# Kernel tuning notes

Measured on AMD Instinct MI355X. Metric: run time of the kernel, lower is better.

Reference implementation:

```python
import jax, jax.numpy as jnp
import numpy as np

B = 4; C = 3; IMG = 256; P = 16; HP = 16; HW = 256
DIM = 512; DEPTH = 6; HEADS = 8; DH = 64
NS = 50; SH = 4; SDH = 64; ITERS = 3; RPD = 128; FF = 2048; N = NS + HW


def _ln(x, g, b):
    m = jnp.mean(x, -1, keepdims=True)
    v = jnp.var(x, -1, keepdims=True)
    return (x - m) * jax.lax.rsqrt(v + 1e-5) * g + b


def _rms(x, g):
    # lucidrains RMSNorm: F.normalize(x, dim=-1) * sqrt(dim) * gamma
    n = jnp.linalg.norm(x, axis=-1, keepdims=True)
    return x / jnp.maximum(n, 1e-12) * (DIM ** 0.5) * g


def setup_inputs() -> dict:
    key = jax.random.key(0)
    ks = iter(jax.random.split(key, 64))
    def W(*s):
        return jax.random.normal(next(ks), s, jnp.float32) * 0.02
    SI = SH * SDH
    d = {}
    d['images'] = jax.random.normal(next(ks), (B, C, IMG, IMG), jnp.float32)
    d['slot_noise'] = jax.random.normal(next(ks), (B, NS, DIM), jnp.float32)
    d['patch_w'] = W(C * P * P, DIM); d['patch_b'] = jnp.zeros((DIM,))
    d['hpos'] = W(HP, DIM); d['wpos'] = W(HP, DIM)
    d['rp_w1'] = W(2, RPD); d['rp_b1'] = jnp.zeros((RPD,))
    d['rp_w2'] = W(RPD, RPD); d['rp_b2'] = jnp.zeros((RPD,))
    d['rp_w3'] = W(RPD, HEADS); d['rp_b3'] = jnp.zeros((HEADS,))
    d['slots_mu'] = W(1, 1, DIM); d['slots_logsigma'] = jnp.zeros((1, 1, DIM))
    d['sa_ln_in_g'] = jnp.ones((DIM,)); d['sa_ln_in_b'] = jnp.zeros((DIM,))
    d['sa_ln_sl_g'] = jnp.ones((DIM,)); d['sa_ln_sl_b'] = jnp.zeros((DIM,))
    d['sa_wq'] = W(DIM, SI); d['sa_bq'] = jnp.zeros((SI,))
    d['sa_wk'] = W(DIM, SI); d['sa_bk'] = jnp.zeros((SI,))
    d['sa_wv'] = W(DIM, SI); d['sa_bv'] = jnp.zeros((SI,))
    d['sa_wo'] = W(SI, DIM); d['sa_bo'] = jnp.zeros((DIM,))
    d['gru_wih'] = W(DIM, 3 * DIM); d['gru_whh'] = W(DIM, 3 * DIM)
    d['gru_bih'] = jnp.zeros((3 * DIM,)); d['gru_bhh'] = jnp.zeros((3 * DIM,))
    d['sa_ln_ff_g'] = jnp.ones((DIM,)); d['sa_ln_ff_b'] = jnp.zeros((DIM,))
    d['sa_mlp_w1'] = W(DIM, DIM); d['sa_mlp_b1'] = jnp.zeros((DIM,))
    d['sa_mlp_w2'] = W(DIM, DIM); d['sa_mlp_b2'] = jnp.zeros((DIM,))
    d['s2c_w'] = W(DIM, 2); d['s2c_b'] = jnp.zeros((2,))
    d['attn_g'] = jnp.ones((DEPTH, DIM))
    d['wq'] = W(DEPTH, DIM, HEADS * DH); d['wk'] = W(DEPTH, DIM, HEADS * DH)
    d['wv'] = W(DEPTH, DIM, HEADS * DH); d['wo'] = W(DEPTH, HEADS * DH, DIM)
    d['ff_g'] = jnp.ones((DEPTH, DIM))
    d['ff_w1'] = W(DEPTH, DIM, FF); d['ff_b1'] = jnp.zeros((DEPTH, FF))
    d['ff_w2'] = W(DEPTH, FF, DIM); d['ff_b2'] = jnp.zeros((DEPTH, DIM))
    d['final_g'] = jnp.ones((DIM,))
    d['pred_w'] = W(DIM, DIM); d['pred_b'] = jnp.zeros((DIM,))
    return d


def reference(images, slot_noise, patch_w, patch_b, hpos, wpos,
              rp_w1, rp_b1, rp_w2, rp_b2, rp_w3, rp_b3,
              slots_mu, slots_logsigma, sa_ln_in_g, sa_ln_in_b, sa_ln_sl_g, sa_ln_sl_b,
              sa_wq, sa_bq, sa_wk, sa_bk, sa_wv, sa_bv, sa_wo, sa_bo,
              gru_wih, gru_whh, gru_bih, gru_bhh, sa_ln_ff_g, sa_ln_ff_b,
              sa_mlp_w1, sa_mlp_b1, sa_mlp_w2, sa_mlp_b2, s2c_w, s2c_b,
              attn_g, wq, wk, wv, wo, ff_g, ff_w1, ff_b1, ff_w2, ff_b2,
              final_g, pred_w, pred_b):
    b = images.shape[0]
    # patchify: b c (h p1) (w p2) -> b h w (p1 p2 c)
    x = images.reshape(b, C, HP, P, HP, P).transpose(0, 2, 4, 3, 5, 1).reshape(b, HP, HP, P * P * C)
    tokens = x @ patch_w + patch_b                     # [b, HP, HP, DIM]
    tokens = tokens + hpos[:, None, :] + wpos[None, :, :]
    tokens = tokens.reshape(b, HW, DIM)
    # --- multi-head slot attention ---
    inp = _ln(tokens, sa_ln_in_g, sa_ln_in_b)
    k = (inp @ sa_wk + sa_bk).reshape(b, HW, SH, SDH).transpose(0, 2, 1, 3)
    v = (inp @ sa_wv + sa_bv).reshape(b, HW, SH, SDH).transpose(0, 2, 1, 3)
    slots = slots_mu + jnp.exp(slots_logsigma) * slot_noise  # [b, NS, DIM]
    scale = SDH ** -0.5
    for _ in range(ITERS):
        prev = slots
        s = _ln(slots, sa_ln_sl_g, sa_ln_sl_b)
        q = (s @ sa_wq + sa_bq).reshape(b, NS, SH, SDH).transpose(0, 2, 1, 3)
        dots = jnp.einsum('bhid,bhjd->bhij', q, k) * scale     # [b, SH, NS, HW]
        attn = jax.nn.softmax(dots, axis=-2) + 1e-8            # softmax over slots
        attn = attn / jnp.sum(attn, -1, keepdims=True)         # weighted mean over inputs
        upd = jnp.einsum('bhij,bhjd->bhid', attn, v)
        upd = upd.transpose(0, 2, 1, 3).reshape(b, NS, SH * SDH) @ sa_wo + sa_bo
        # GRUCell(updates, prev_slots)
        gx = upd @ gru_wih + gru_bih
        gh = prev @ gru_whh + gru_bhh
        xr, xz, xn = jnp.split(gx, 3, -1)
        hr, hz, hn = jnp.split(gh, 3, -1)
        r = jax.nn.sigmoid(xr + hr)
        z = jax.nn.sigmoid(xz + hz)
        nn_ = jnp.tanh(xn + r * hn)
        slots = (1 - z) * nn_ + z * prev
        slots = slots + (jax.nn.relu(_ln(slots, sa_ln_ff_g, sa_ln_ff_b) @ sa_mlp_w1 + sa_mlp_b1) @ sa_mlp_w2 + sa_mlp_b2)
    objects = slots
    slot_coords = objects @ s2c_w + s2c_b              # [b, NS, 2]
    # --- relative position MLP bias (slots coords + patch grid) ---
    g = jnp.arange(HP, dtype=jnp.float32)
    grid = jnp.stack(jnp.meshgrid(g, g, indexing='ij'), -1).reshape(HW, 2)
    coords = jnp.concatenate([slot_coords, jnp.broadcast_to(grid, (b, HW, 2))], axis=1)  # [b, N, 2]
    rel = coords[:, :, None, :] - coords[:, None, :, :]   # [b, N, N, 2]
    hmid = jax.nn.silu(rel @ rp_w1 + rp_b1)
    hmid = jax.nn.silu(hmid @ rp_w2 + rp_b2)
    bias = jnp.transpose(hmid @ rp_w3 + rp_b3, (0, 3, 1, 2))  # [b, HEADS, N, N]
    # --- transformer with per-layer rel-pos bias ---
    x = jnp.concatenate([objects, tokens], axis=1)     # [b, N, DIM]
    ascale = DH ** -0.5
    for l in range(DEPTH):
        h = _rms(x, attn_g[l])
        qh = (h @ wq[l]).reshape(b, N, HEADS, DH).transpose(0, 2, 1, 3)
        kh = (h @ wk[l]).reshape(b, N, HEADS, DH).transpose(0, 2, 1, 3)
        vh = (h @ wv[l]).reshape(b, N, HEADS, DH).transpose(0, 2, 1, 3)
        sim = jnp.einsum('bhid,bhjd->bhij', qh, kh) * ascale + bias
        a = jax.nn.softmax(sim, -1)
        o = jnp.einsum('bhij,bhjd->bhid', a, vh).transpose(0, 2, 1, 3).reshape(b, N, HEADS * DH) @ wo[l]
        x = x + o
        h = _rms(x, ff_g[l])
        x = x + (jax.nn.gelu(h @ ff_w1[l] + ff_b1[l]) @ ff_w2[l] + ff_b2[l])
    x = _rms(x, final_g)
    return x[:, NS:] @ pred_w + pred_b                 # [b, HW, DIM]
```

## Files before the change

### kernel.cpp

```cpp
#include <hip/hip_runtime.h>
#include <hip/hip_bf16.h>

typedef __hip_bfloat16 bf16;
typedef short short8v __attribute__((ext_vector_type(8)));
typedef float float4v __attribute__((ext_vector_type(4)));

static __device__ __forceinline__ float b2f(bf16 x){ return __bfloat162float(x); }

static __device__ __forceinline__ float ldin(const void* p, size_t i, bool isbf) {
  return isbf ? b2f(((const bf16*)p)[i]) : ((const float*)p)[i];
}

static __device__ __forceinline__ unsigned short f2bu(float f) {
  bf16 h = __float2bfloat16(f);
  return *reinterpret_cast<unsigned short*>(&h);
}

#define CDIV(a,b) (((a)+(b)-1)/(b))

#define NB   4
#define NSL  50
#define HWT  256
#define NT   306
#define DIM  512
#define NH   8
#define FF   2048
#define RPP  28100
#define PCH  56200

static __device__ __forceinline__ void rp_decode(int q, int& i, int& j) {
  if (q < 15300) { i = q / NT; j = q % NT; }
  else { int r = q - 15300; i = NSL + r / NSL; j = r % NSL; }
}

__global__ void detect_k(const void* p, int* flag) {
  const unsigned short* u = (const unsigned short*)p;
  int t = threadIdx.x;
  int e = (u[t] >> 7) & 0xFF;
  __shared__ int anybad;
  if (t == 0) anybad = 0;
  __syncthreads();
  if (e >= 0x88) atomicOr(&anybad, 1);
  __syncthreads();
  if (t == 0) *flag = anybad ? 0 : 1;
}

struct WtArgs {
  const void* W[17];
  unsigned long long wto[17];
  int K[17], N[17];
  int base[18];
};

__global__ __launch_bounds__(256) void wtrans_all_k(WtArgs a, unsigned short* __restrict__ WT,
                                                    const int* __restrict__ flagp) {
  const bool isbf = *flagp != 0;
  int bid = blockIdx.x;
  int idx = 0;
#pragma unroll
  for (int i = 1; i < 17; ++i) if (bid >= a.base[i]) idx = i;
  int t0 = bid - a.base[idx];
  const int K = a.K[idx], N = a.N[idx];
  const int tilesN = N >> 6;
  const int perLayer = tilesN * (K >> 6);
  const int layer = t0 / perLayer, rem = t0 % perLayer;
  const int n0 = (rem % tilesN) * 64, k0 = (rem / tilesN) * 64;
  const void* W = a.W[idx];
  unsigned short* dst0 = WT + a.wto[idx];
  const size_t slice = (size_t)K * N * layer;

  __shared__ unsigned short S[64 * 72];
  int t = threadIdx.x;
  int kk = t >> 4, nn = (t & 15) * 4;
#pragma unroll
  for (int r = 0; r < 4; ++r) {
    int k = k0 + kk + r * 16;
    unsigned short v[4];
    if (isbf) {
      ushort4 u = *(const ushort4*)((const unsigned short*)W + slice + (size_t)k * N + n0 + nn);
      v[0]=u.x; v[1]=u.y; v[2]=u.z; v[3]=u.w;
    } else {
      float4 f = *(const float4*)((const float*)W + slice + (size_t)k * N + n0 + nn);
      v[0]=f2bu(f.x); v[1]=f2bu(f.y); v[2]=f2bu(f.z); v[3]=f2bu(f.w);
    }
#pragma unroll
    for (int i = 0; i < 4; ++i) S[(nn + i) * 72 + kk + r * 16] = v[i];
  }
  __syncthreads();
  int nr = t >> 2, kc = (t & 3) * 16;
  short8v s0 = *(const short8v*)&S[nr * 72 + kc];
  short8v s1 = *(const short8v*)&S[nr * 72 + kc + 8];
  unsigned short* dst = dst0 + slice + (size_t)(n0 + nr) * K + k0 + kc;
  *(short8v*)dst = s0;
  *(short8v*)(dst + 8) = s1;
}

#define LDK 72
static __device__ __forceinline__ void gemm_body2(
    const void* __restrict__ A, int aty,
    const unsigned short* __restrict__ WT,
    const void* __restrict__ bias, size_t boff,
    void* __restrict__ C, int oty,
    int M, int N, int K, int kbeg, int kend,
    int act, int mode, int spec,
    const void* __restrict__ p0, const void* __restrict__ p1,
    bool isbf)
{
  __shared__ unsigned short As[64 * LDK];
  __shared__ unsigned short Bs[64 * LDK];
  const int tid = threadIdx.x;
  const int lane = tid & 63, wave = tid >> 6;
  const int quad = lane >> 4, ti = lane & 15;
  const int wm = (wave & 1) * 32, wn = (wave >> 1) * 32;
  const int bm = blockIdx.y * 64, bn = blockIdx.x * 64;
  const int srow = tid >> 2, sch = (tid & 3) * 16;

  unsigned short ha[16], hb[16];
  const int gm = bm + srow;
  const bool aok = gm < M;
  const unsigned short* Abf = (const unsigned short*)A + (size_t)gm * K;
  const float*          Af  = (const float*)A + (size_t)gm * K;
  const unsigned short* Bp  = WT + (size_t)(bn + srow) * K;

  auto fetchA = [&](int k0) {
    if (aok) {
      if (aty) {
        const ushort4* ap = (const ushort4*)(Abf + k0 + sch);
#pragma unroll
        for (int i = 0; i < 4; ++i) {
          ushort4 u = ap[i];
          ha[i*4+0]=u.x; ha[i*4+1]=u.y; ha[i*4+2]=u.z; ha[i*4+3]=u.w;
        }
      } else {
        const float4* ap = (const float4*)(Af + k0 + sch);
#pragma unroll
        for (int i = 0; i < 4; ++i) {
          float4 f = ap[i];
          ha[i*4+0]=f2bu(f.x); ha[i*4+1]=f2bu(f.y); ha[i*4+2]=f2bu(f.z); ha[i*4+3]=f2bu(f.w);
        }
      }
    } else {
#pragma unroll
      for (int i = 0; i < 16; ++i) ha[i] = 0;
    }
  };
  auto fetchB = [&](int k0) {
    const ushort4* bp = (const ushort4*)(Bp + k0 + sch);
#pragma unroll
    for (int i = 0; i < 4; ++i) {
      ushort4 u = bp[i];
      hb[i*4+0]=u.x; hb[i*4+1]=u.y; hb[i*4+2]=u.z; hb[i*4+3]=u.w;
    }
  };

  float4v acc00 = {0,0,0,0}, acc01 = {0,0,0,0}, acc10 = {0,0,0,0}, acc11 = {0,0,0,0};
  fetchA(kbeg); fetchB(kbeg);
  for (int k0 = kbeg; k0 < kend; k0 += 64) {
    *(short8v*)&As[srow * LDK + sch]     = *(short8v*)ha;
    *(short8v*)&As[srow * LDK + sch + 8] = *(short8v*)(ha + 8);
    *(short8v*)&Bs[srow * LDK + sch]     = *(short8v*)hb;
    *(short8v*)&Bs[srow * LDK + sch + 8] = *(short8v*)(hb + 8);
    __syncthreads();
    if (k0 + 64 < kend) { fetchA(k0 + 64); fetchB(k0 + 64); }
#pragma unroll
    for (int ks = 0; ks < 2; ++ks) {
      short8v a0 = *reinterpret_cast<const short8v*>(&As[(wm + ti)      * LDK + ks * 32 + quad * 8]);
      short8v a1 = *reinterpret_cast<const short8v*>(&As[(wm + 16 + ti) * LDK + ks * 32 + quad * 8]);
      short8v b0 = *reinterpret_cast<const short8v*>(&Bs[(wn + ti)      * LDK + ks * 32 + quad * 8]);
      short8v b1 = *reinterpret_cast<const short8v*>(&Bs[(wn + 16 + ti) * LDK + ks * 32 + quad * 8]);
      acc00 = __builtin_amdgcn_mfma_f32_16x16x32_bf16(a0, b0, acc00, 0, 0, 0);
      acc01 = __builtin_amdgcn_mfma_f32_16x16x32_bf16(a0, b1, acc01, 0, 0, 0);
      acc10 = __builtin_amdgcn_mfma_f32_16x16x32_bf16(a1, b0, acc10, 0, 0, 0);
      acc11 = __builtin_amdgcn_mfma_f32_16x16x32_bf16(a1, b1, acc11, 0, 0, 0);
    }
    __syncthreads();
  }

  float4v accs[2][2] = {{acc00, acc01}, {acc10, acc11}};
#pragma unroll
  for (int mi = 0; mi < 2; ++mi) {
#pragma unroll
    for (int ni = 0; ni < 2; ++ni) {
      int row0 = bm + wm + mi * 16 + quad * 4;
      int col  = bn + wn + ni * 16 + ti;
      float bv = (bias && kbeg == 0) ? ldin(bias, boff + col, isbf) : 0.f;
#pragma unroll
      for (int r = 0; r < 4; ++r) {
        int row = row0 + r;
        if (row >= M) continue;
        float v = accs[mi][ni][r] + bv;
        if (act == 1) v = fmaxf(v, 0.f);
        else if (act == 2) {
          float u = 0.7978845608028654f * (v + 0.044715f * v * v * v);
          v = 0.5f * v * (1.f + tanhf(u));
        } else if (act == 3) {
          v = v / (1.f + expf(-v));
        }
        if (spec == 2 && kbeg == 0) {
          int hh = (row >> 4) & 15, ww = row & 15;
          v += ldin(p0, hh * N + col, isbf) + ldin(p1, ww * N + col, isbf);
        }
        if (spec == 1) {
          int b_ = row / NT, n_ = row % NT;
          if (n_ >= NSL) {
            size_t oi = ((size_t)(b_ * HWT + (n_ - NSL))) * N + col;
            if (isbf) ((bf16*)C)[oi] = __float2bfloat16(v);
            else      ((float*)C)[oi] = v;
          }
        } else {
          size_t idx = (size_t)row * N + col;
          if (oty) ((bf16*)C)[idx] = __float2bfloat16(v);
          else {
            float* Cf = (float*)C;
            if (mode == 2) atomicAdd(&Cf[idx], v);
            else if (mode == 1) Cf[idx] += v;
            else Cf[idx] = v;
          }
        }
      }
    }
  }
}

__global__ __launch_bounds__(256) void gemm_mfma(
    const void* A, int aty, const unsigned short* WT, size_t woff,
    const void* bias, size_t boff, void* C, int oty,
    int M, int N, int K, int act, int accum, int zsplit,
    int spec, const void* p0, const void* p1, const int* __restrict__ flagp)
{
  int ksz = K / zsplit;
  int kbeg = blockIdx.z * ksz;
  int mode = zsplit > 1 ? 2 : (accum ? 1 : 0);
  gemm_body2(A, aty, WT + woff, bias, boff, C, oty, M, N, K, kbeg, kbeg + ksz,
             act, mode, spec, p0, p1, *flagp != 0);
}

__global__ __launch_bounds__(256) void gemm_mfma_tri(
    const void* A, int aty, const unsigned short* WT, size_t o0, size_t o1, size_t o2,
    void* C0, void* C1, void* C2, int oty, int M, int N, int K,
    const int* __restrict__ flagp)
{
  size_t o = blockIdx.z == 0 ? o0 : (blockIdx.z == 1 ? o1 : o2);
  void* C = blockIdx.z == 0 ? C0 : (blockIdx.z == 1 ? C1 : C2);
  gemm_body2(A, aty, WT + o, nullptr, 0, C, oty, M, N, K, 0, K, 0, 0, 0,
             nullptr, nullptr, *flagp != 0);
}

__global__ __launch_bounds__(256) void gemm_mfma_duo(
    const void* A0, const void* A1, int aty, const unsigned short* WT, size_t o0, size_t o1,
    const void* bias0, const void* bias1, void* C0, void* C1, int oty,
    int M, int N, int K, const int* __restrict__ flagp)
{
  const void* A = blockIdx.z ? A1 : A0;
  size_t o = blockIdx.z ? o1 : o0;
  const void* bias = blockIdx.z ? bias1 : bias0;
  void* C = blockIdx.z ? C1 : C0;
  gemm_body2(A, aty, WT + o, bias, 0, C, oty, M, N, K, 0, K, 0, 0, 0,
             nullptr, nullptr, *flagp != 0);
}

__global__ void coords_k(const float* __restrict__ slots, const void* __restrict__ w,
                         const void* __restrict__ bv, float* __restrict__ coords,
                         const int* __restrict__ flagp) {
  const bool isbf = *flagp != 0;
  __shared__ float r0[256], r1[256];
  int blk = blockIdx.x, t = threadIdx.x;
  if (blk < 200) {
    int b = blk / 50, n = blk % 50;
    const float* x = slots + (size_t)blk * DIM;
    float v0 = x[t], v1 = x[t + 256];
    float a0 = v0 * ldin(w, 2 * t, isbf)     + v1 * ldin(w, 2 * (t + 256), isbf);
    float a1 = v0 * ldin(w, 2 * t + 1, isbf) + v1 * ldin(w, 2 * (t + 256) + 1, isbf);
    r0[t] = a0; r1[t] = a1;
    __syncthreads();
    for (int o = 128; o > 0; o >>= 1) {
      if (t < o) { r0[t] += r0[t + o]; r1[t] += r1[t + o]; }
      __syncthreads();
    }
    if (t == 0) {
      coords[((size_t)b * NT + n) * 2]     = r0[0] + ldin(bv, 0, isbf);
      coords[((size_t)b * NT + n) * 2 + 1] = r1[0] + ldin(bv, 1, isbf);
    }
  } else {
#pragma unroll
    for (int s = 0; s < 4; ++s) {
      int i = t + 256 * s;
      int b = i >> 8, tt = i & 255;
      coords[((size_t)b * NT + NSL + tt) * 2]     = (float)(tt >> 4);
      coords[((size_t)b * NT + NSL + tt) * 2 + 1] = (float)(tt & 15);
    }
  }
}

__global__ void patchify_k(const void* __restrict__ img, unsigned short* __restrict__ xp,
                           const int* __restrict__ flagp) {
  const bool isbf = *flagp != 0;
  int i = blockIdx.x * 256 + threadIdx.x;
  if (i >= NB * HWT * 768) return;
  int col = i % 768, row = i / 768;
  int c = col % 3, p2 = (col / 3) & 15, p1 = col / 48;
  int w = row & 15, h = (row >> 4) & 15, b = row >> 8;
  xp[i] = f2bu(ldin(img, (((size_t)(b * 3 + c) * 256 + h * 16 + p1) * 256) + w * 16 + p2, isbf));
}

__global__ void ln512_k(const float* __restrict__ X, const void* __restrict__ g,
                        const void* __restrict__ b, unsigned short* __restrict__ Y,
                        const int* __restrict__ flagp) {
  const bool isbf = *flagp != 0;
  int row = blockIdx.x, t = threadIdx.x;
  const float* x = X + (size_t)row * DIM;
  float v0 = x[t], v1 = x[t + 256];
  __shared__ float rs[256], rq[256];
  rs[t] = v0 + v1; rq[t] = v0 * v0 + v1 * v1;
  __syncthreads();
  for (int o = 128; o > 0; o >>= 1) {
    if (t < o) { rs[t] += rs[t + o]; rq[t] += rq[t + o]; }
    __syncthreads();
  }
  float mean = rs[0] * (1.f / 512.f);
  float var  = rq[0] * (1.f / 512.f) - mean * mean;
  float inv  = rsqrtf(var + 1e-5f);
  unsigned short* y = Y + (size_t)row * DIM;
  y[t]       = f2bu((v0 - mean) * inv * ldin(g, t, isbf)       + ldin(b, t, isbf));
  y[t + 256] = f2bu((v1 - mean) * inv * ldin(g, t + 256, isbf) + ldin(b, t + 256, isbf));
}

__global__ void rms512_k(const float* __restrict__ X, const void* __restrict__ g,
                         int goff, unsigned short* __restrict__ Y, const int* __restrict__ flagp) {
  const bool isbf = *flagp != 0;
  int row = blockIdx.x, t = threadIdx.x;
  const float* x = X + (size_t)row * DIM;
  float v0 = x[t], v1 = x[t + 256];
  __shared__ float rq[256];
  rq[t] = v0 * v0 + v1 * v1;
  __syncthreads();
  for (int o = 128; o > 0; o >>= 1) {
    if (t < o) rq[t] += rq[t + o];
    __syncthreads();
  }
  float nrm = sqrtf(rq[0]);
  float sc = 22.62741699796952f / fmaxf(nrm, 1e-12f);
  unsigned short* y = Y + (size_t)row * DIM;
  y[t]       = f2bu(v0 * sc * ldin(g, goff + t, isbf));
  y[t + 256] = f2bu(v1 * sc * ldin(g, goff + t + 256, isbf));
}

__global__ void slots_init_k(const void* __restrict__ mu, const void* __restrict__ ls,
                             const void* __restrict__ noise, float* __restrict__ slots,
                             const int* __restrict__ flagp) {
  const bool isbf = *flagp != 0;
  int i = blockIdx.x * 256 + threadIdx.x;
  if (i >= NB * NSL * DIM) return;
  int d = i & 511;
  slots[i] = ldin(mu, d, isbf) + expf(ldin(ls, d, isbf)) * ldin(noise, i, isbf);
}

__global__ void slot_dots_k(const float* __restrict__ q, const float* __restrict__ k,
                            float* __restrict__ dots) {
  int blk = blockIdx.x;
  int i = blk % 50, h = (blk / 50) & 3, b = blk / 200;
  int j = threadIdx.x;
  __shared__ float qs[64];
  if (threadIdx.x < 64) qs[threadIdx.x] = q[((size_t)(b * 50 + i)) * 256 + h * 64 + threadIdx.x];
  __syncthreads();
  const float* kr = k + ((size_t)(b * 256 + j)) * 256 + h * 64;
  float s = 0.f;
#pragma unroll 8
  for (int d = 0; d < 64; ++d) s = fmaf(qs[d], kr[d], s);
  dots[(((size_t)(b * 4 + h) * 50) + i) * 256 + j] = s * 0.125f;
}

__global__ __launch_bounds__(256) void sm_renorm_k(float* __restrict__ att) {
  __shared__ float S[NSL * 257];
  const int t = threadIdx.x;
  float* base = att + (size_t)blockIdx.x * (NSL * HWT);
  float v[NSL];
#pragma unroll
  for (int i = 0; i < NSL; ++i) v[i] = base[i * HWT + t];
  float m = -1e30f;
#pragma unroll
  for (int i = 0; i < NSL; ++i) m = fmaxf(m, v[i]);
  float s = 0.f;
#pragma unroll
  for (int i = 0; i < NSL; ++i) { float e = __expf(v[i] - m); v[i] = e; s += e; }
  float inv = 1.f / s;
#pragma unroll
  for (int i = 0; i < NSL; ++i) S[i * 257 + t] = fmaf(v[i], inv, 1e-8f);
  __syncthreads();
  const int w = t >> 6, l = t & 63;
  for (int r = w; r < NSL; r += 4) {
    float a0 = S[r * 257 + l],        a1 = S[r * 257 + 64 + l];
    float a2 = S[r * 257 + 128 + l],  a3 = S[r * 257 + 192 + l];
    float s4 = a0 + a1 + a2 + a3;
#pragma unroll
    for (int o = 1; o < 64; o <<= 1) s4 += __shfl_xor(s4, o);
    float inv2 = 1.f / s4;
    base[r * HWT + l]       = a0 * inv2;
    base[r * HWT + 64 + l]  = a1 * inv2;
    base[r * HWT + 128 + l] = a2 * inv2;
    base[r * HWT + 192 + l] = a3 * inv2;
  }
}

__global__ void slot_upd_k(const float* __restrict__ attn, const float* __restrict__ v,
                           float* __restrict__ upd) {
  int bi = blockIdx.x;
  int b = bi / 50, i = bi % 50;
  int t = threadIdx.x, h = t >> 6;
  const float* arow = attn + ((size_t)((b * 4 + h) * 50) + i) * 256;
  float s = 0.f;
  for (int j = 0; j < 256; ++j) s = fmaf(arow[j], v[((size_t)(b * 256 + j)) * 256 + t], s);
  upd[(size_t)bi * 256 + t] = s;
}

__global__ void gru_k(const float* __restrict__ gx, const float* __restrict__ gh,
                      float* __restrict__ slots) {
  int i = blockIdx.x * 256 + threadIdx.x;
  if (i >= NB * NSL * DIM) return;
  int row = i >> 9, d = i & 511;
  size_t b3 = (size_t)row * 1536;
  float xr = gx[b3 + d], xz = gx[b3 + 512 + d], xn = gx[b3 + 1024 + d];
  float hr = gh[b3 + d], hz = gh[b3 + 512 + d], hn = gh[b3 + 1024 + d];
  float r = 1.f / (1.f + expf(-(xr + hr)));
  float z = 1.f / (1.f + expf(-(xz + hz)));
  float n = tanhf(xn + r * hn);
  float prev = slots[i];
  slots[i] = (1.f - z) * n + z * prev;
}

__global__ void relpos_table_k(const void* w1, const void* b1, const void* w2,
                               const void* b2, const void* w3, const void* b3,
                               float* __restrict__ tab, const int* __restrict__ flagp) {
  const bool isbf = *flagp != 0;
  int blk = blockIdx.x;
  float r0 = (float)(blk / 31 - 15), r1 = (float)(blk % 31 - 15);
  int t = threadIdx.x;
  __shared__ float h1[128], h2[128];
  float a = fmaf(r0, ldin(w1, t, isbf), fmaf(r1, ldin(w1, 128 + t, isbf), ldin(b1, t, isbf)));
  h1[t] = a / (1.f + expf(-a));
  __syncthreads();
  float s = ldin(b2, t, isbf);
#pragma unroll 4
  for (int k = 0; k < 128; ++k) s = fmaf(h1[k], ldin(w2, k * 128 + t, isbf), s);
  h2[t] = s / (1.f + expf(-s));
  __syncthreads();
  if (t < 8) {
    float o = ldin(b3, t, isbf);
#pragma unroll 4
    for (int k = 0; k < 128; ++k) o = fmaf(h2[k], ldin(w3, k * 8 + t, isbf), o);
    tab[blk * 8 + t] = o;
  }
}

__global__ void bias_fill_k(const float* __restrict__ tab, float* __restrict__ bias) {
  int i = blockIdx.x * 256 + threadIdx.x;
  if (i >= NB * NH * HWT * HWT) return;
  int jj = i & 255, ii = (i >> 8) & 255, h = (i >> 16) & 7, b = i >> 19;
  int di = (ii >> 4) - (jj >> 4) + 15;
  int dj = (ii & 15) - (jj & 15) + 15;
  bias[(((size_t)(b * NH + h) * NT) + NSL + ii) * NT + NSL + jj] = tab[(di * 31 + dj) * 8 + h];
}

__global__ void rp_l1_k(const float* __restrict__ coords, const void* w1, const void* b1,
                        unsigned short* __restrict__ H, int pbase, int pcount,
                        const int* __restrict__ flagp) {
  const bool isbf = *flagp != 0;
  int idx = blockIdx.x * 256 + threadIdx.x;
  if (idx >= pcount * 128) return;
  int pl = idx >> 7, u = idx & 127;
  int p = pbase + pl;
  int q = p % RPP, bb = p / RPP;
  int ii, jj;
  rp_decode(q, ii, jj);
  float r0 = coords[(bb * NT + ii) * 2]     - coords[(bb * NT + jj) * 2];
  float r1 = coords[(bb * NT + ii) * 2 + 1] - coords[(bb * NT + jj) * 2 + 1];
  float a = fmaf(r0, ldin(w1, u, isbf), fmaf(r1, ldin(w1, 128 + u, isbf), ldin(b1, u, isbf)));
  H[(size_t)pl * 128 + u] = f2bu(a / (1.f + expf(-a)));
}

__global__ __launch_bounds__(256) void rp_l3_k(
    const unsigned short* __restrict__ H2, const void* w3, const void* b3,
    float* __restrict__ bias, int pbase, int pcount, const int* __restrict__ flagp) {
  const bool isbf = *flagp != 0;
  __shared__ float W3s[8 * 132];
  int t = threadIdx.x;
  for (int e = t; e < 1024; e += 256) {
    int k = e >> 3, hh = e & 7;
    W3s[hh * 132 + k] = ldin(w3, e, isbf);
  }
  __syncthreads();
  int pl = blockIdx.x * 32 + (t >> 3), hh = t & 7;
  if (pl >= pcount) return;
  int p = pbase + pl;
  int q = p % RPP, bb = p / RPP;
  int ii, jj;
  rp_decode(q, ii, jj);
  float s = ldin(b3, hh, isbf);
  const unsigned short* hrow = H2 + (size_t)pl * 128;
  const float* wrow = &W3s[hh * 132];
#pragma unroll 8
  for (int k4 = 0; k4 < 32; ++k4) {
    ushort4 h4 = *(const ushort4*)(hrow + k4 * 4);
    float4  w4 = *(const float4*)(wrow + k4 * 4);
    s = fmaf(b2f(*reinterpret_cast<bf16*>(&h4.x)), w4.x, s);
    s = fmaf(b2f(*reinterpret_cast<bf16*>(&h4.y)), w4.y, s);
    s = fmaf(b2f(*reinterpret_cast<bf16*>(&h4.z)), w4.z, s);
    s = fmaf(b2f(*reinterpret_cast<bf16*>(&h4.w)), w4.w, s);
  }
  bias[((size_t)(bb * NH + hh) * NT + ii) * NT + jj] = s;
}

__global__ void build_x_k(const float* __restrict__ slots, const float* __restrict__ tok,
                          float* __restrict__ x) {
  int i = blockIdx.x * 256 + threadIdx.x;
  if (i >= NB * NT * DIM) return;
  int d = i & 511, n = (i >> 9) % NT, b = i / (NT * DIM);
  x[i] = (n < NSL) ? slots[((size_t)(b * NSL + n)) * DIM + d]
                   : tok[((size_t)(b * HWT + (n - NSL))) * DIM + d];
}

__global__ __launch_bounds__(256) void attn_fused_k(
    const unsigned short* __restrict__ Qb, const unsigned short* __restrict__ Kb,
    const unsigned short* __restrict__ Vb, const float* __restrict__ bias,
    unsigned short* __restrict__ Ob)
{
  const int bh = blockIdx.y, b = bh >> 3, h = bh & 7;
  const int i0 = blockIdx.x * 32;
  __shared__ unsigned short Qs[32 * 72];
  __shared__ unsigned short Ks[64 * 72];
  __shared__ float S[32 * 332];
  unsigned short* P = (unsigned short*)S;

  const int tid = threadIdx.x;
  const int lane = tid & 63, wave = tid >> 6, quad = lane >> 4, ti = lane & 15;
  const int mi = wave & 1, nh = wave >> 1;

  {
    int r = tid >> 3, c = (tid & 7) * 8;
    int gi = i0 + r;
    ushort4 u0 = {0,0,0,0}, u1 = {0,0,0,0};
    if (gi < NT) {
      const ushort4* p = (const ushort4*)(Qb + ((size_t)(b * NT + gi)) * DIM + h * 64 + c);
      u0 = p[0]; u1 = p[1];
    }
    *(ushort4*)&Qs[r * 72 + c] = u0;
    *(ushort4*)&Qs[r * 72 + c + 4] = u1;
  }

  for (int kt = 0; kt < 5; ++kt) {
    __syncthreads();
    {
      int kr = tid >> 2, c = (tid & 3) * 16;
      int gj = kt * 64 + kr;
      ushort4 v[4] = {{0,0,0,0},{0,0,0,0},{0,0,0,0},{0,0,0,0}};
      if (gj < NT) {
        const ushort4* p = (const ushort4*)(Kb + ((size_t)(b * NT + gj)) * DIM + h * 64 + c);
#pragma unroll
        for (int i = 0; i < 4; ++i) v[i] = p[i];
      }
#pragma unroll
      for (int i = 0; i < 4; ++i) *(ushort4*)&Ks[kr * 72 + c + i * 4] = v[i];
    }
    __syncthreads();
#pragma unroll
    for (int ntl = 0; ntl < 2; ++ntl) {
      int nt = nh * 2 + ntl;
      float4v acc = {0,0,0,0};
#pragma unroll
      for (int ks = 0; ks < 2; ++ks) {
        short8v a  = *(const short8v*)&Qs[(mi * 16 + ti) * 72 + ks * 32 + quad * 8];
        short8v bb = *(const short8v*)&Ks[(nt * 16 + ti) * 72 + ks * 32 + quad * 8];
        acc = __builtin_amdgcn_mfma_f32_16x16x32_bf16(a, bb, acc, 0, 0, 0);
      }
      int colL = kt * 64 + nt * 16 + ti;
      int row0 = mi * 16 + quad * 4;
#pragma unroll
      for (int r = 0; r < 4; ++r) {
        int row_g = i0 + row0 + r;
        float val;
        if (colL < NT) {
          float bv = (row_g < NT) ? bias[((size_t)bh * NT + row_g) * NT + colL] : 0.f;
          val = acc[r] * 0.125f + bv;
        } else val = -1e30f;
        S[(row0 + r) * 332 + colL] = val;
      }
    }
  }
  __syncthreads();

  {
    int rl = tid >> 3, sub = tid & 7;
    float sv[40];
#pragma unroll
    for (int k = 0; k < 40; ++k) sv[k] = S[rl * 332 + sub + k * 8];
    float m = -1e30f;
#pragma unroll
    for (int k = 0; k < 40; ++k) m = fmaxf(m, sv[k]);
    m = fmaxf(m, __shfl_xor(m, 1));
    m = fmaxf(m, __shfl_xor(m, 2));
    m = fmaxf(m, __shfl_xor(m, 4));
    float s = 0.f;
#pragma unroll
    for (int k = 0; k < 40; ++k) { float e = __expf(sv[k] - m); sv[k] = e; s += e; }
    s += __shfl_xor(s, 1);
    s += __shfl_xor(s, 2);
    s += __shfl_xor(s, 4);
    float inv = 1.f / s;
    __syncthreads();
#pragma unroll
    for (int k = 0; k < 40; ++k) P[rl * 664 + sub + k * 8] = f2bu(sv[k] * inv);
  }

  float4v oacc[2] = {{0,0,0,0},{0,0,0,0}};
  for (int vt = 0; vt < 5; ++vt) {
    __syncthreads();
    {
      int key = tid & 63, d0 = (tid >> 6) * 16;
      int gj = vt * 64 + key;
      unsigned short hv[16];
      if (gj < NT) {
        const ushort4* p = (const ushort4*)(Vb + ((size_t)(b * NT + gj)) * DIM + h * 64 + d0);
#pragma unroll
        for (int i = 0; i < 4; ++i) {
          ushort4 u = p[i];
          hv[i*4+0]=u.x; hv[i*4+1]=u.y; hv[i*4+2]=u.z; hv[i*4+3]=u.w;
        }
      } else {
#pragma unroll
        for (int i = 0; i < 16; ++i) hv[i] = 0;
      }
#pragma unroll
      for (int i = 0; i < 16; ++i) Ks[(d0 + i) * 72 + key] = hv[i];
    }
    __syncthreads();
#pragma unroll
    for (int ntl = 0; ntl < 2; ++ntl) {
      int nt = nh * 2 + ntl;
#pragma unroll
      for (int ks = 0; ks < 2; ++ks) {
        short8v a  = *(const short8v*)&P[(mi * 16 + ti) * 664 + vt * 64 + ks * 32 + quad * 8];
        short8v bb = *(const short8v*)&Ks[(nt * 16 + ti) * 72 + ks * 32 + quad * 8];
        oacc[ntl] = __builtin_amdgcn_mfma_f32_16x16x32_bf16(a, bb, oacc[ntl], 0, 0, 0);
      }
    }
  }

#pragma unroll
  for (int ntl = 0; ntl < 2; ++ntl) {
    int dim = nh * 32 + ntl * 16 + ti;
#pragma unroll
    for (int r = 0; r < 4; ++r) {
      int row_g = i0 + mi * 16 + quad * 4 + r;
      if (row_g < NT)
        Ob[((size_t)(b * NT + row_g)) * DIM + h * 64 + dim] = f2bu(oacc[ntl][r]);
    }
  }
}

extern "C" void kernel_launch(void* const* d_in, const int* in_sizes, int n_in,
                              void* d_out, int out_size, void* d_ws, size_t ws_size,
                              hipStream_t stream) {
  const void* images        = d_in[0];
  const void* slot_noise    = d_in[1];
  const void* patch_w       = d_in[2];
  const void* patch_b       = d_in[3];
  const void* hpos          = d_in[4];
  const void* wpos          = d_in[5];
  const void* rp_w1         = d_in[6];
  const void* rp_b1         = d_in[7];
  const void* rp_w2         = d_in[8];
  const void* rp_b2         = d_in[9];
  const void* rp_w3         = d_in[10];
  const void* rp_b3         = d_in[11];
  const void* slots_mu      = d_in[12];
  const void* slots_logsig  = d_in[13];
  const void* sa_ln_in_g    = d_in[14];
  const void* sa_ln_in_b    = d_in[15];
  const void* sa_ln_sl_g    = d_in[16];
  const void* sa_ln_sl_b    = d_in[17];
  const void* sa_wq         = d_in[18];
  const void* sa_bq         = d_in[19];
  const void* sa_wk         = d_in[20];
  const void* sa_bk         = d_in[21];
  const void* sa_wv         = d_in[22];
  const void* sa_bv         = d_in[23];
  const void* sa_wo         = d_in[24];
  const void* sa_bo         = d_in[25];
  const void* gru_wih       = d_in[26];
  const void* gru_whh       = d_in[27];
  const void* gru_bih       = d_in[28];
  const void* gru_bhh       = d_in[29];
  const void* sa_ln_ff_g    = d_in[30];
  const void* sa_ln_ff_b    = d_in[31];
  const void* sa_mlp_w1     = d_in[32];
  const void* sa_mlp_b1     = d_in[33];
  const void* sa_mlp_w2     = d_in[34];
  const void* sa_mlp_b2     = d_in[35];
  const void* s2c_w         = d_in[36];
  const void* s2c_b         = d_in[37];
  const void* attn_g        = d_in[38];
  const void* wq            = d_in[39];
  const void* wk            = d_in[40];
  const void* wv            = d_in[41];
  const void* wo            = d_in[42];
  const void* ff_g          = d_in[43];
  const void* ff_w1         = d_in[44];
  const void* ff_b1         = d_in[45];
  const void* ff_w2         = d_in[46];
  const void* ff_b2         = d_in[47];
  const void* final_g       = d_in[48];
  const void* pred_w        = d_in[49];
  const void* pred_b        = d_in[50];

  float* ws = (float*)d_ws;
  int* FLAG = (int*)ws;
  size_t off = 16;
  auto alloc = [&](size_t n) { float* p = ws + off; off += (n + 15) & ~(size_t)15; return p; };
  float* TOK   = alloc((size_t)NB * HWT * DIM);
  unsigned short* INPB = (unsigned short*)alloc((size_t)NB * HWT * DIM / 2);
  float* KB    = alloc((size_t)NB * HWT * 256);
  float* VB    = alloc((size_t)NB * HWT * 256);
  float* SLOTS = alloc((size_t)NB * NSL * DIM);
  unsigned short* SLNB = (unsigned short*)alloc((size_t)NB * NSL * DIM / 2);
  float* QB    = alloc((size_t)NB * NSL * 256);
  float* ATT   = alloc((size_t)NB * 4 * NSL * HWT);
  float* UPD   = alloc((size_t)NB * NSL * 256);
  float* UPDP  = alloc((size_t)NB * NSL * DIM);
  unsigned short* HIDSB = (unsigned short*)alloc((size_t)NB * NSL * DIM / 2);
  float* CRD   = alloc((size_t)NB * NT * 2);
  float* TAB   = alloc((size_t)961 * 8);
  float* BIAS  = alloc((size_t)NB * NH * NT * NT);
  float* X     = alloc((size_t)NB * NT * DIM);
  unsigned short* HBB  = (unsigned short*)alloc((size_t)NB * NT * DIM / 2);
  unsigned short* QHB  = (unsigned short*)alloc((size_t)NB * NT * DIM / 2);
  unsigned short* KHB  = (unsigned short*)alloc((size_t)NB * NT * DIM / 2);
  unsigned short* VHB  = (unsigned short*)alloc((size_t)NB * NT * DIM / 2);
  float* SIM   = alloc((size_t)NB * NH * NT * NT);
  unsigned short* OBB  = (unsigned short*)alloc((size_t)NB * NT * DIM / 2);
  unsigned short* FFHB = (unsigned short*)alloc((size_t)NB * NT * FF / 2);
  float* OUTT  = alloc((size_t)NB * NT * DIM);
  unsigned short* XPB = (unsigned short*)OUTT;
  float* GX = SIM;
  float* GH = SIM + (size_t)NB * NSL * 1536;
  const size_t oPatch = 0;
  const size_t oKw    = oPatch + (size_t)512 * 768;
  const size_t oVw    = oKw    + (size_t)256 * 512;
  const size_t oQw    = oVw    + (size_t)256 * 512;
  const size_t oWo    = oQw    + (size_t)256 * 512;
  const size_t oGih   = oWo    + (size_t)512 * 256;
  const size_t oGhh   = oGih   + (size_t)1536 * 512;
  const size_t oMlp1  = oGhh   + (size_t)1536 * 512;
  const size_t oMlp2  = oMlp1  + (size_t)512 * 512;
  const size_t oRp2   = oMlp2  + (size_t)512 * 512;
  const size_t oWq    = oRp2   + (size_t)128 * 128;
  const size_t oWk    = oWq    + (size_t)6 * 512 * 512;
  const size_t oWv    = oWk    + (size_t)6 * 512 * 512;
  const size_t oWol   = oWv    + (size_t)6 * 512 * 512;
  const size_t oFf1   = oWol   + (size_t)6 * 512 * 512;
  const size_t oFf2   = oFf1   + (size_t)6 * 512 * 2048;
  const size_t oPred  = oFf2   + (size_t)6 * 2048 * 512;
  const size_t wtTotal = oPred + (size_t)512 * 512;
  unsigned short* WTS = (unsigned short*)alloc((wtTotal + 1) / 2);
  (void)ws_size; (void)in_sizes; (void)n_in; (void)out_size;

#define GEMMM(A_, ATY_, WOFF_, BIAS_, BOFF_, C_, OTY_, M_, N_, K_, ACT_, ACC_, ZS_, SPEC_, P0_, P1_) \
  gemm_mfma<<<dim3((N_)/64, CDIV((M_),64), (ZS_)), 256, 0, stream>>>( \
      A_, ATY_, WTS, (size_t)(WOFF_), BIAS_, (size_t)(BOFF_), C_, OTY_, M_, N_, K_, ACT_, ACC_, ZS_, \
      SPEC_, P0_, P1_, FLAG)

  const int MROW = NB * NT;
  const int MS   = NB * NSL;

  detect_k<<<1, 256, 0, stream>>>(images, FLAG);
  {
    WtArgs a;
    const void* Wp[17] = { patch_w, sa_wk, sa_wv, sa_wq, sa_wo, gru_wih, gru_whh,
                           sa_mlp_w1, sa_mlp_w2, rp_w2, wq, wk, wv, wo, ff_w1, ff_w2, pred_w };
    const size_t Oo[17] = { oPatch, oKw, oVw, oQw, oWo, oGih, oGhh,
                            oMlp1, oMlp2, oRp2, oWq, oWk, oWv, oWol, oFf1, oFf2, oPred };
    const int Kk[17] = {768,512,512,512,256,512,512,512,512,128,512,512,512,512,512,2048,512};
    const int Nn[17] = {512,256,256,256,512,1536,1536,512,512,128,512,512,512,512,2048,512,512};
    const int Ll[17] = {1,1,1,1,1,1,1,1,1,1,6,6,6,6,6,6,1};
    int acc = 0;
    for (int i = 0; i < 17; ++i) {
      a.W[i] = Wp[i]; a.wto[i] = Oo[i]; a.K[i] = Kk[i]; a.N[i] = Nn[i];
      a.base[i] = acc;
      acc += Ll[i] * (Kk[i] >> 6) * (Nn[i] >> 6);
    }
    a.base[17] = acc;
    wtrans_all_k<<<acc, 256, 0, stream>>>(a, WTS, FLAG);
  }

  patchify_k<<<CDIV(NB*HWT*768, 256), 256, 0, stream>>>(images, XPB, FLAG);
  GEMMM(XPB, 1, oPatch, patch_b, 0, TOK, 0, NB*HWT, DIM, 768, 0, 0, 1, 2, hpos, wpos);

  ln512_k<<<NB*HWT, 256, 0, stream>>>(TOK, sa_ln_in_g, sa_ln_in_b, INPB, FLAG);
  gemm_mfma_duo<<<dim3(4, 16, 2), 256, 0, stream>>>(
      INPB, INPB, 1, WTS, oKw, oVw, sa_bk, sa_bv, KB, VB, 0, NB*HWT, 256, DIM, FLAG);
  slots_init_k<<<CDIV(NB*NSL*DIM, 256), 256, 0, stream>>>(slots_mu, slots_logsig, slot_noise, SLOTS, FLAG);

  for (int it = 0; it < 3; ++it) {
    ln512_k<<<MS, 256, 0, stream>>>(SLOTS, sa_ln_sl_g, sa_ln_sl_b, SLNB, FLAG);
    GEMMM(SLNB, 1, oQw, sa_bq, 0, QB, 0, MS, 256, DIM, 0, 0, 1, 0, nullptr, nullptr);
    slot_dots_k<<<NB*4*NSL, 256, 0, stream>>>(QB, KB, ATT);
    sm_renorm_k<<<16, 256, 0, stream>>>(ATT);
    slot_upd_k<<<MS, 256, 0, stream>>>(ATT, VB, UPD);
    GEMMM(UPD, 0, oWo, sa_bo, 0, UPDP, 0, MS, DIM, 256, 0, 0, 1, 0, nullptr, nullptr);
    gemm_mfma_duo<<<dim3(24, 4, 2), 256, 0, stream>>>(
        UPDP, SLOTS, 0, WTS, oGih, oGhh, gru_bih, gru_bhh, GX, GH, 0, MS, 1536, DIM, FLAG);
    gru_k<<<CDIV(NB*NSL*DIM, 256), 256, 0, stream>>>(GX, GH, SLOTS);
    ln512_k<<<MS, 256, 0, stream>>>(SLOTS, sa_ln_ff_g, sa_ln_ff_b, SLNB, FLAG);
    GEMMM(SLNB, 1, oMlp1, sa_mlp_b1, 0, HIDSB, 1, MS, DIM, DIM, 1, 0, 1, 0, nullptr, nullptr);
    GEMMM(HIDSB, 1, oMlp2, sa_mlp_b2, 0, SLOTS, 0, MS, DIM, DIM, 0, 1, 1, 0, nullptr, nullptr);
  }

  coords_k<<<201, 256, 0, stream>>>(SLOTS, s2c_w, s2c_b, CRD, FLAG);
  relpos_table_k<<<961, 128, 0, stream>>>(rp_w1, rp_b1, rp_w2, rp_b2, rp_w3, rp_b3, TAB, FLAG);
  bias_fill_k<<<CDIV(NB*NH*HWT*HWT, 256), 256, 0, stream>>>(TAB, BIAS);
  {
    unsigned short* H1 = HBB;
    unsigned short* H2 = HBB + (size_t)PCH * 128;
    for (int c = 0; c < 2; ++c) {
      int pb = c * PCH;
      rp_l1_k<<<CDIV(PCH*128, 256), 256, 0, stream>>>(CRD, rp_w1, rp_b1, H1, pb, PCH, FLAG);
      GEMMM(H1, 1, oRp2, rp_b2, 0, H2, 1, PCH, 128, 128, 3, 0, 1, 0, nullptr, nullptr);
      rp_l3_k<<<CDIV(PCH,32), 256, 0, stream>>>(H2, rp_w3, rp_b3, BIAS, pb, PCH, FLAG);
    }
  }

  build_x_k<<<CDIV(NB*NT*DIM, 256), 256, 0, stream>>>(SLOTS, TOK, X);
  for (int l = 0; l < 6; ++l) {
    size_t lw = (size_t)l * 512 * 512;
    rms512_k<<<MROW, 256, 0, stream>>>(X, attn_g, l * DIM, HBB, FLAG);
    gemm_mfma_tri<<<dim3(8, 20, 3), 256, 0, stream>>>(
        HBB, 1, WTS, oWq + lw, oWk + lw, oWv + lw, QHB, KHB, VHB, 1, MROW, DIM, DIM, FLAG);
    attn_fused_k<<<dim3(10, NB*NH), 256, 0, stream>>>(QHB, KHB, VHB, BIAS, OBB);
    GEMMM(OBB, 1, oWol + lw, (const void*)nullptr, 0, X, 0, MROW, DIM, DIM, 0, 1, 2, 0, nullptr, nullptr);
    rms512_k<<<MROW, 256, 0, stream>>>(X, ff_g, l * DIM, HBB, FLAG);
    GEMMM(HBB, 1, oFf1 + (size_t)l * 512 * 2048, ff_b1, l * FF, FFHB, 1, MROW, FF, DIM, 2, 0, 1, 0, nullptr, nullptr);
    GEMMM(FFHB, 1, oFf2 + (size_t)l * 2048 * 512, ff_b2, l * DIM, X, 0, MROW, DIM, FF, 0, 1, 4, 0, nullptr, nullptr);
  }

  rms512_k<<<MROW, 256, 0, stream>>>(X, final_g, 0, HBB, FLAG);
  GEMMM(HBB, 1, oPred, pred_b, 0, d_out, 0, MROW, DIM, DIM, 0, 0, 1, 1, nullptr, nullptr);

#undef GEMMM
}
```

Measured before the change: 1.186 ms.

## Add 128x64 MFMA GEMM tile and use it for transformer GEMMs

Adds a GEMM body with 128-row tiles, where each wave computes a 64x32 sub-tile so B fragments are reused across four A fragments. The QKV, output-projection, FF1, FF2 and relpos GEMMs switch to it, which halves the grid's M dimension. The patch-embedding GEMM also becomes a 3-way K-split with atomic accumulation into a pre-zeroed buffer. The larger tile cuts LDS and global traffic per MFMA but uses more registers and launches fewer blocks, which may lower occupancy for M=1224. The epilogue is factored into a shared helper.

```diff
diff --git a/kernel.cpp b/kernel.cpp
--- a/kernel.cpp
+++ b/kernel.cpp
@@ -93,6 +93,52 @@
   unsigned short* dst = dst0 + slice + (size_t)(n0 + nr) * K + k0 + kc;
   *(short8v*)dst = s0;
   *(short8v*)(dst + 8) = s1;
+}
+
+static __device__ __forceinline__ void gemm_epi(
+    float4v accv, int row0, int col,
+    const void* __restrict__ bias, size_t boff,
+    void* __restrict__ C, int oty,
+    int M, int N, int kbeg,
+    int act, int mode, int spec,
+    const void* __restrict__ p0, const void* __restrict__ p1,
+    bool isbf)
+{
+  float bv = (bias && kbeg == 0) ? ldin(bias, boff + col, isbf) : 0.f;
+#pragma unroll
+  for (int r = 0; r < 4; ++r) {
+    int row = row0 + r;
+    if (row >= M) continue;
+    float v = accv[r] + bv;
+    if (act == 1) v = fmaxf(v, 0.f);
+    else if (act == 2) {
+      float u = 0.7978845608028654f * (v + 0.044715f * v * v * v);
+      v = 0.5f * v * (1.f + tanhf(u));
+    } else if (act == 3) {
+      v = v / (1.f + expf(-v));
+    }
+    if (spec == 2 && kbeg == 0) {
+      int hh = (row >> 4) & 15, ww = row & 15;
+      v += ldin(p0, hh * N + col, isbf) + ldin(p1, ww * N + col, isbf);
+    }
+    if (spec == 1) {
+      int b_ = row / NT, n_ = row % NT;
+      if (n_ >= NSL) {
+        size_t oi = ((size_t)(b_ * HWT + (n_ - NSL))) * N + col;
+        if (isbf) ((bf16*)C)[oi] = __float2bfloat16(v);
+        else      ((float*)C)[oi] = v;
+      }
+    } else {
+      size_t idx = (size_t)row * N + col;
+      if (oty) ((bf16*)C)[idx] = __float2bfloat16(v);
+      else {
+        float* Cf = (float*)C;
+        if (mode == 2) atomicAdd(&Cf[idx], v);
+        else if (mode == 1) Cf[idx] += v;
+        else Cf[idx] = v;
+      }
+    }
+  }
 }
 
 #define LDK 72
@@ -178,48 +224,106 @@
 
   float4v accs[2][2] = {{acc00, acc01}, {acc10, acc11}};
 #pragma unroll
-  for (int mi = 0; mi < 2; ++mi) {
-#pragma unroll
-    for (int ni = 0; ni < 2; ++ni) {
-      int row0 = bm + wm + mi * 16 + quad * 4;
-      int col  = bn + wn + ni * 16 + ti;
-      float bv = (bias && kbeg == 0) ? ldin(bias, boff + col, isbf) : 0.f;
-#pragma unroll
-      for (int r = 0; r < 4; ++r) {
-        int row = row0 + r;
-        if (row >= M) continue;
-        float v = accs[mi][ni][r] + bv;
-        if (act == 1) v = fmaxf(v, 0.f);
-        else if (act == 2) {
-          float u = 0.7978845608028654f * (v + 0.044715f * v * v * v);
-          v = 0.5f * v * (1.f + tanhf(u));
-        } else if (act == 3) {
-          v = v / (1.f + expf(-v));
+  for (int mi = 0; mi < 2; ++mi)
+#pragma unroll
+    for (int ni = 0; ni < 2; ++ni)
+      gemm_epi(accs[mi][ni], bm + wm + mi * 16 + quad * 4, bn + wn + ni * 16 + ti,
+               bias, boff, C, oty, M, N, kbeg, act, mode, spec, p0, p1, isbf);
+}
+
+static __device__ __forceinline__ void gemm_body128(
+    const void* __restrict__ A, int aty,
+    const unsigned short* __restrict__ WT,
+    const void* __restrict__ bias, size_t boff,
+    void* __restrict__ C, int oty,
+    int M, int N, int K, int kbeg, int kend,
+    int act, int mode, int spec,
+    const void* __restrict__ p0, const void* __restrict__ p1,
+    bool isbf)
+{
+  __shared__ unsigned short As[128 * LDK];
+  __shared__ unsigned short Bs[64 * LDK];
+  const int tid = threadIdx.x;
+  const int lane = tid & 63, wave = tid >> 6;
+  const int quad = lane >> 4, ti = lane & 15;
+  const int wm = (wave & 1) * 64, wn = (wave >> 1) * 32;
+  const int bm = blockIdx.y * 128, bn = blockIdx.x * 64;
+  const int srA = tid >> 1, scA = (tid & 1) * 32;
+  const int srB = tid >> 2, scB = (tid & 3) * 16;
+
+  unsigned short ha[32], hb[16];
+  const int gmA = bm + srA;
+  const bool aok = gmA < M;
+  const unsigned short* Abf = (const unsigned short*)A + (size_t)gmA * K;
+  const float*          Af  = (const float*)A + (size_t)gmA * K;
+  const unsigned short* Bp  = WT + (size_t)(bn + srB) * K;
+
+  auto fetchA = [&](int k0) {
+    if (aok) {
+      if (aty) {
+        const ushort4* ap = (const ushort4*)(Abf + k0 + scA);
+#pragma unroll
+        for (int i = 0; i < 8; ++i) {
+          ushort4 u = ap[i];
+          ha[i*4+0]=u.x; ha[i*4+1]=u.y; ha[i*4+2]=u.z; ha[i*4+3]=u.w;
         }
-        if (spec == 2 && kbeg == 0) {
-          int hh = (row >> 4) & 15, ww = row & 15;
-          v += ldin(p0, hh * N + col, isbf) + ldin(p1, ww * N + col, isbf);
-        }
-        if (spec == 1) {
-          int b_ = row / NT, n_ = row % NT;
-          if (n_ >= NSL) {
-            size_t oi = ((size_t)(b_ * HWT + (n_ - NSL))) * N + col;
-            if (isbf) ((bf16*)C)[oi] = __float2bfloat16(v);
-            else      ((float*)C)[oi] = v;
-          }
-        } else {
-          size_t idx = (size_t)row * N + col;
-          if (oty) ((bf16*)C)[idx] = __float2bfloat16(v);
-          else {
-            float* Cf = (float*)C;
-            if (mode == 2) atomicAdd(&Cf[idx], v);
-            else if (mode == 1) Cf[idx] += v;
-            else Cf[idx] = v;
-          }
+      } else {
+        const float4* ap = (const float4*)(Af + k0 + scA);
+#pragma unroll
+        for (int i = 0; i < 8; ++i) {
+          float4 f = ap[i];
+          ha[i*4+0]=f2bu(f.x); ha[i*4+1]=f2bu(f.y); ha[i*4+2]=f2bu(f.z); ha[i*4+3]=f2bu(f.w);
         }
       }
-    }
-  }
+    } else {
+#pragma unroll
+      for (int i = 0; i < 32; ++i) ha[i] = 0;
+    }
+  };
+  auto fetchB = [&](int k0) {
+    const ushort4* bp = (const ushort4*)(Bp + k0 + scB);
+#pragma unroll
+    for (int i = 0; i < 4; ++i) {
+      ushort4 u = bp[i];
+      hb[i*4+0]=u.x; hb[i*4+1]=u.y; hb[i*4+2]=u.z; hb[i*4+3]=u.w;
+    }
+  };
+
+  float4v acc[4][2];
+#pragma unroll
+  for (int mi = 0; mi < 4; ++mi) {
+    acc[mi][0] = (float4v){0,0,0,0};
+    acc[mi][1] = (float4v){0,0,0,0};
+  }
+  fetchA(kbeg); fetchB(kbeg);
+  for (int k0 = kbeg; k0 < kend; k0 += 64) {
+#pragma unroll
+    for (int i = 0; i < 4; ++i)
+      *(short8v*)&As[srA * LDK + scA + i * 8] = *(short8v*)(ha + i * 8);
+    *(short8v*)&Bs[srB * LDK + scB]     = *(short8v*)hb;
+    *(short8v*)&Bs[srB * LDK + scB + 8] = *(short8v*)(hb + 8);
+    __syncthreads();
+    if (k0 + 64 < kend) { fetchA(k0 + 64); fetchB(k0 + 64); }
+#pragma unroll
+    for (int ks = 0; ks < 2; ++ks) {
+      short8v b0 = *reinterpret_cast<const short8v*>(&Bs[(wn + ti)      * LDK + ks * 32 + quad * 8]);
+      short8v b1 = *reinterpret_cast<const short8v*>(&Bs[(wn + 16 + ti) * LDK + ks * 32 + quad * 8]);
+#pragma unroll
+      for (int mi = 0; mi < 4; ++mi) {
+        short8v a = *reinterpret_cast<const short8v*>(&As[(wm + mi * 16 + ti) * LDK + ks * 32 + quad * 8]);
+        acc[mi][0] = __builtin_amdgcn_mfma_f32_16x16x32_bf16(a, b0, acc[mi][0], 0, 0, 0);
+        acc[mi][1] = __builtin_amdgcn_mfma_f32_16x16x32_bf16(a, b1, acc[mi][1], 0, 0, 0);
+      }
+    }
+    __syncthreads();
+  }
+
+#pragma unroll
+  for (int mi = 0; mi < 4; ++mi)
+#pragma unroll
+    for (int ni = 0; ni < 2; ++ni)
+      gemm_epi(acc[mi][ni], bm + wm + mi * 16 + quad * 4, bn + wn + ni * 16 + ti,
+               bias, boff, C, oty, M, N, kbeg, act, mode, spec, p0, p1, isbf);
 }
 
 __global__ __launch_bounds__(256) void gemm_mfma(
@@ -235,15 +339,28 @@
              act, mode, spec, p0, p1, *flagp != 0);
 }
 
-__global__ __launch_bounds__(256) void gemm_mfma_tri(
+__global__ __launch_bounds__(256) void gemm_mfma128(
+    const void* A, int aty, const unsigned short* WT, size_t woff,
+    const void* bias, size_t boff, void* C, int oty,
+    int M, int N, int K, int act, int accum, int zsplit,
+    int spec, const void* p0, const void* p1, const int* __restrict__ flagp)
+{
+  int ksz = K / zsplit;
+  int kbeg = blockIdx.z * ksz;
+  int mode = zsplit > 1 ? 2 : (accum ? 1 : 0);
+  gemm_body128(A, aty, WT + woff, bias, boff, C, oty, M, N, K, kbeg, kbeg + ksz,
+               act, mode, spec, p0, p1, *flagp != 0);
+}
+
+__global__ __launch_bounds__(256) void gemm_mfma_tri128(
     const void* A, int aty, const unsigned short* WT, size_t o0, size_t o1, size_t o2,
     void* C0, void* C1, void* C2, int oty, int M, int N, int K,
     const int* __restrict__ flagp)
 {
   size_t o = blockIdx.z == 0 ? o0 : (blockIdx.z == 1 ? o1 : o2);
   void* C = blockIdx.z == 0 ? C0 : (blockIdx.z == 1 ? C1 : C2);
-  gemm_body2(A, aty, WT + o, nullptr, 0, C, oty, M, N, K, 0, K, 0, 0, 0,
-             nullptr, nullptr, *flagp != 0);
+  gemm_body128(A, aty, WT + o, nullptr, 0, C, oty, M, N, K, 0, K, 0, 0, 0,
+               nullptr, nullptr, *flagp != 0);
 }
 
 __global__ __launch_bounds__(256) void gemm_mfma_duo(
@@ -768,6 +885,11 @@
       A_, ATY_, WTS, (size_t)(WOFF_), BIAS_, (size_t)(BOFF_), C_, OTY_, M_, N_, K_, ACT_, ACC_, ZS_, \
       SPEC_, P0_, P1_, FLAG)
 
+#define GEMM128(A_, ATY_, WOFF_, BIAS_, BOFF_, C_, OTY_, M_, N_, K_, ACT_, ACC_, ZS_, SPEC_, P0_, P1_) \
+  gemm_mfma128<<<dim3((N_)/64, CDIV((M_),128), (ZS_)), 256, 0, stream>>>( \
+      A_, ATY_, WTS, (size_t)(WOFF_), BIAS_, (size_t)(BOFF_), C_, OTY_, M_, N_, K_, ACT_, ACC_, ZS_, \
+      SPEC_, P0_, P1_, FLAG)
+
   const int MROW = NB * NT;
   const int MS   = NB * NSL;
 
@@ -792,7 +914,8 @@
   }
 
   patchify_k<<<CDIV(NB*HWT*768, 256), 256, 0, stream>>>(images, XPB, FLAG);
-  GEMMM(XPB, 1, oPatch, patch_b, 0, TOK, 0, NB*HWT, DIM, 768, 0, 0, 1, 2, hpos, wpos);
+  hipMemsetAsync(TOK, 0, (size_t)NB * HWT * DIM * sizeof(float), stream);
+  GEMM128(XPB, 1, oPatch, patch_b, 0, TOK, 0, NB*HWT, DIM, 768, 0, 0, 3, 2, hpos, wpos);
 
   ln512_k<<<NB*HWT, 256, 0, stream>>>(TOK, sa_ln_in_g, sa_ln_in_b, INPB, FLAG);
   gemm_mfma_duo<<<dim3(4, 16, 2), 256, 0, stream>>>(
@@ -823,7 +946,7 @@
     for (int c = 0; c < 2; ++c) {
       int pb = c * PCH;
       rp_l1_k<<<CDIV(PCH*128, 256), 256, 0, stream>>>(CRD, rp_w1, rp_b1, H1, pb, PCH, FLAG);
-      GEMMM(H1, 1, oRp2, rp_b2, 0, H2, 1, PCH, 128, 128, 3, 0, 1, 0, nullptr, nullptr);
+      GEMM128(H1, 1, oRp2, rp_b2, 0, H2, 1, PCH, 128, 128, 3, 0, 1, 0, nullptr, nullptr);
       rp_l3_k<<<CDIV(PCH,32), 256, 0, stream>>>(H2, rp_w3, rp_b3, BIAS, pb, PCH, FLAG);
     }
   }
@@ -832,17 +955,18 @@
   for (int l = 0; l < 6; ++l) {
     size_t lw = (size_t)l * 512 * 512;
     rms512_k<<<MROW, 256, 0, stream>>>(X, attn_g, l * DIM, HBB, FLAG);
-    gemm_mfma_tri<<<dim3(8, 20, 3), 256, 0, stream>>>(
+    gemm_mfma_tri128<<<dim3(8, CDIV(MROW,128), 3), 256, 0, stream>>>(
         HBB, 1, WTS, oWq + lw, oWk + lw, oWv + lw, QHB, KHB, VHB, 1, MROW, DIM, DIM, FLAG);
     attn_fused_k<<<dim3(10, NB*NH), 256, 0, stream>>>(QHB, KHB, VHB, BIAS, OBB);
-    GEMMM(OBB, 1, oWol + lw, (const void*)nullptr, 0, X, 0, MROW, DIM, DIM, 0, 1, 2, 0, nullptr, nullptr);
+    GEMM128(OBB, 1, oWol + lw, (const void*)nullptr, 0, X, 0, MROW, DIM, DIM, 0, 1, 2, 0, nullptr, nullptr);
     rms512_k<<<MROW, 256, 0, stream>>>(X, ff_g, l * DIM, HBB, FLAG);
-    GEMMM(HBB, 1, oFf1 + (size_t)l * 512 * 2048, ff_b1, l * FF, FFHB, 1, MROW, FF, DIM, 2, 0, 1, 0, nullptr, nullptr);
-    GEMMM(FFHB, 1, oFf2 + (size_t)l * 2048 * 512, ff_b2, l * DIM, X, 0, MROW, DIM, FF, 0, 1, 4, 0, nullptr, nullptr);
+    GEMM128(HBB, 1, oFf1 + (size_t)l * 512 * 2048, ff_b1, l * FF, FFHB, 1, MROW, FF, DIM, 2, 0, 1, 0, nullptr, nullptr);
+    GEMM128(FFHB, 1, oFf2 + (size_t)l * 2048 * 512, ff_b2, l * DIM, X, 0, MROW, DIM, FF, 0, 1, 4, 0, nullptr, nullptr);
   }
 
   rms512_k<<<MROW, 256, 0, stream>>>(X, final_g, 0, HBB, FLAG);
   GEMMM(HBB, 1, oPred, pred_b, 0, d_out, 0, MROW, DIM, DIM, 0, 0, 1, 1, nullptr, nullptr);
 
 #undef GEMMM
-}
+#undef GEMM128
+}
```

After: 1.316 ms. 1.11x slower.
